# Performance work log

Hardware: AMD Instinct MI355X
Metric: run time of the kernel (lower is better)

The kernel has to match this reference:

```python
import jax, jax.numpy as jnp
import numpy as np

EPS = 1e-08


def setup_inputs() -> dict:
    key = jax.random.key(0)
    student_output = jax.random.normal(key, (8192, 1024), dtype=jnp.float32)
    return {"student_output": student_output}


def reference(student_output) -> jnp.ndarray:
    # F.normalize(p=2, dim=-1, eps=EPS): x / max(||x||_2, eps)
    x = student_output.astype(jnp.float32)
    norm = jnp.linalg.norm(x, axis=-1, keepdims=True)
    x = x / jnp.maximum(norm, EPS)

    n = x.shape[0]
    # full similarity matrix with diagonal masked to -1.0 (self-sim excluded)
    sim = x @ x.T  # [N, N]
    sim = jnp.where(jnp.eye(n, dtype=bool), jnp.float32(-1.0), sim)
    indices = jnp.argmax(sim, axis=1)  # nearest neighbor per row

    # torch.nn.PairwiseDistance(2, eps): ||x1 - x2 + eps||_2 along feature dim
    diff = x - x[indices] + EPS
    distances = jnp.sqrt(jnp.sum(diff * diff, axis=-1))

    return -jnp.mean(jnp.log(distances + EPS))
```

## Files before the change

### kernel.cpp

```cpp
#include <hip/hip_runtime.h>
#include <stdint.h>

#define N 8192
#define DIM 1024
#define EPSF 1e-8f
#define BK 64
#define NBLK 64
#define NTRI 2080

typedef __attribute__((ext_vector_type(4))) float f32x4;
typedef __attribute__((ext_vector_type(8))) short s16x8;

__device__ inline unsigned short f2bf(float f) {
  unsigned u = __float_as_uint(f);
  unsigned r = (u + 0x7FFFu + ((u >> 16) & 1u)) >> 16;
  return (unsigned short)r;
}

__device__ inline unsigned encf(float f) {
  unsigned u = __float_as_uint(f);
  return (u & 0x80000000u) ? ~u : (u | 0x80000000u);
}

#define XB_OFF   0
#define INV_OFF  16777216
#define KEY_OFF  16809984
#define PART_OFF 16875520

__global__ __launch_bounds__(256)
void k_norm(const float* __restrict__ x, unsigned short* __restrict__ xb,
            float* __restrict__ invn, unsigned long long* __restrict__ keys) {
  int row = blockIdx.x, t = threadIdx.x;
  const float4* xr = (const float4*)(x + (size_t)row * DIM);
  float4 v = xr[t];
  float ss = v.x * v.x + v.y * v.y + v.z * v.z + v.w * v.w;
#pragma unroll
  for (int o = 32; o > 0; o >>= 1) ss += __shfl_down(ss, o, 64);
  __shared__ float red[4];
  __shared__ float sinv;
  if ((t & 63) == 0) red[t >> 6] = ss;
  __syncthreads();
  if (t == 0) {
    float s = red[0] + red[1] + red[2] + red[3];
    float inv = 1.0f / fmaxf(sqrtf(s), EPSF);
    sinv = inv;
    invn[row] = inv;
    keys[row] = 0ull;
  }
  __syncthreads();
  float inv = sinv;
  ushort4 o4;
  o4.x = f2bf(v.x * inv);
  o4.y = f2bf(v.y * inv);
  o4.z = f2bf(v.z * inv);
  o4.w = f2bf(v.w * inv);
  ((ushort4*)(xb + (size_t)row * DIM))[t] = o4;
}

__global__ __launch_bounds__(256)
void k_sim(const unsigned short* __restrict__ xb, unsigned long long* __restrict__ keys) {
  int b = blockIdx.x;
  int bi = (int)((129.0f - sqrtf(16641.0f - 8.0f * (float)b)) * 0.5f);
  while ((bi + 1) * (129 - (bi + 1)) / 2 <= b) ++bi;
  while (bi * (129 - bi) / 2 > b) --bi;
  int bj = bi + (b - bi * (129 - bi) / 2);

  __shared__ unsigned short sA[128 * BK];
  __shared__ unsigned short sB[128 * BK];
  const int t = threadIdx.x, lane = t & 63, wv = t >> 6;
  const int wr = wv >> 1, wc = wv & 1;
  const int hi = lane >> 4, lo = lane & 15;
  const int rowBase = bi * 128, colBase = bj * 128;

  const f32x4 fzero = {0.f, 0.f, 0.f, 0.f};
  f32x4 acc[4][4];
#pragma unroll
  for (int i = 0; i < 4; ++i)
#pragma unroll
    for (int j = 0; j < 4; ++j) acc[i][j] = fzero;

  const int w8 = wv * 8 + (lane >> 3);
  const int cch = lane & 7;

  for (int kt = 0; kt < DIM / BK; ++kt) {
    const unsigned short* gA = xb + (size_t)rowBase * DIM + kt * BK;
    const unsigned short* gB = xb + (size_t)colBase * DIM + kt * BK;
#pragma unroll
    for (int rd = 0; rd < 4; ++rd) {
      int r = rd * 32 + w8;
      int c = cch ^ (r & 7);
      __builtin_amdgcn_global_load_lds(
          (const __attribute__((address_space(1))) void*)(gA + (size_t)r * DIM + c * 8),
          (__attribute__((address_space(3))) void*)(&sA[rd * 2048 + wv * 512]),
          16, 0, 0);
      __builtin_amdgcn_global_load_lds(
          (const __attribute__((address_space(1))) void*)(gB + (size_t)r * DIM + c * 8),
          (__attribute__((address_space(3))) void*)(&sB[rd * 2048 + wv * 512]),
          16, 0, 0);
    }
    __syncthreads();
#pragma unroll
    for (int kk = 0; kk < 2; ++kk) {
      s16x8 af[4], bf[4];
#pragma unroll
      for (int mi = 0; mi < 4; ++mi) {
        int r = wr * 64 + mi * 16 + lo;
        int c = (kk * 4 + hi) ^ (r & 7);
        af[mi] = *(const s16x8*)(&sA[r * BK + c * 8]);
      }
#pragma unroll
      for (int ni = 0; ni < 4; ++ni) {
        int r = wc * 64 + ni * 16 + lo;
        int c = (kk * 4 + hi) ^ (r & 7);
        bf[ni] = *(const s16x8*)(&sB[r * BK + c * 8]);
      }
#pragma unroll
      for (int mi = 0; mi < 4; ++mi)
#pragma unroll
        for (int ni = 0; ni < 4; ++ni)
          acc[mi][ni] = __builtin_amdgcn_mfma_f32_16x16x32_bf16(af[mi], bf[ni], acc[mi][ni], 0, 0, 0);
    }
    __syncthreads();
  }

#pragma unroll
  for (int mi = 0; mi < 4; ++mi) {
#pragma unroll
    for (int reg = 0; reg < 4; ++reg) {
      int grow = rowBase + wr * 64 + mi * 16 + hi * 4 + reg;
      float best = -10.0f;
      int bcol = 0;
#pragma unroll
      for (int ni = 0; ni < 4; ++ni) {
        int gcol = colBase + wc * 64 + ni * 16 + lo;
        float v = acc[mi][ni][reg];
        v = (gcol == grow) ? -10.0f : v;
        if (v > best || (v == best && gcol < bcol)) { best = v; bcol = gcol; }
      }
#pragma unroll
      for (int m = 1; m < 16; m <<= 1) {
        float ov = __shfl_xor(best, m, 64);
        int oc = __shfl_xor(bcol, m, 64);
        if (ov > best || (ov == best && oc < bcol)) { best = ov; bcol = oc; }
      }
      if (lo == 0) {
        unsigned long long key = ((unsigned long long)encf(best) << 32) | (unsigned)(~bcol);
        atomicMax(&keys[grow], key);
      }
    }
  }

  if (bi != bj) {
#pragma unroll
    for (int ni = 0; ni < 4; ++ni) {
      int gcol = colBase + wc * 64 + ni * 16 + lo;
      float best = -10.0f;
      int brow = 0;
#pragma unroll
      for (int mi = 0; mi < 4; ++mi)
#pragma unroll
        for (int reg = 0; reg < 4; ++reg) {
          int grow = rowBase + wr * 64 + mi * 16 + hi * 4 + reg;
          float v = acc[mi][ni][reg];
          if (v > best || (v == best && grow < brow)) { best = v; brow = grow; }
        }
#pragma unroll
      for (int m = 16; m < 64; m <<= 1) {
        float ov = __shfl_xor(best, m, 64);
        int oc = __shfl_xor(brow, m, 64);
        if (ov > best || (ov == best && oc < brow)) { best = ov; brow = oc; }
      }
      if (hi == 0) {
        unsigned long long key = ((unsigned long long)encf(best) << 32) | (unsigned)(~brow);
        atomicMax(&keys[gcol], key);
      }
    }
  }
}

__global__ __launch_bounds__(256)
void k_dist(const float* __restrict__ x, const float* __restrict__ invn,
            const unsigned long long* __restrict__ keys, float* __restrict__ part) {
  int row = blockIdx.x, t = threadIdx.x;
  unsigned long long key = keys[row];
  int nb = (int)(~(unsigned)key);
  float ia = invn[row], ib = invn[nb];
  float4 a = ((const float4*)(x + (size_t)row * DIM))[t];
  float4 b = ((const float4*)(x + (size_t)nb * DIM))[t];
  float d0 = a.x * ia - b.x * ib + EPSF;
  float d1 = a.y * ia - b.y * ib + EPSF;
  float d2 = a.z * ia - b.z * ib + EPSF;
  float d3 = a.w * ia - b.w * ib + EPSF;
  float ss = d0 * d0 + d1 * d1 + d2 * d2 + d3 * d3;
#pragma unroll
  for (int o = 32; o > 0; o >>= 1) ss += __shfl_down(ss, o, 64);
  __shared__ float red[4];
  if ((t & 63) == 0) red[t >> 6] = ss;
  __syncthreads();
  if (t == 0) {
    float s = red[0] + red[1] + red[2] + red[3];
    part[row] = logf(sqrtf(s) + EPSF);
  }
}

__global__ __launch_bounds__(1024)
void k_final(const float* __restrict__ part, float* __restrict__ out) {
  int t = threadIdx.x;
  float s = 0.0f;
#pragma unroll
  for (int i = 0; i < N / 1024; ++i) s += part[t + i * 1024];
#pragma unroll
  for (int o = 32; o > 0; o >>= 1) s += __shfl_down(s, o, 64);
  __shared__ float red[16];
  if ((t & 63) == 0) red[t >> 6] = s;
  __syncthreads();
  if (t == 0) {
    float tot = 0.0f;
#pragma unroll
    for (int i = 0; i < 16; ++i) tot += red[i];
    out[0] = -tot / (float)N;
  }
}

extern "C" void kernel_launch(void* const* d_in, const int* in_sizes, int n_in,
                              void* d_out, int out_size, void* d_ws, size_t ws_size,
                              hipStream_t stream) {
  const float* x = (const float*)d_in[0];
  float* out = (float*)d_out;
  char* ws = (char*)d_ws;
  unsigned short* xb = (unsigned short*)(ws + XB_OFF);
  float* invn = (float*)(ws + INV_OFF);
  unsigned long long* keys = (unsigned long long*)(ws + KEY_OFF);
  float* part = (float*)(ws + PART_OFF);

  k_norm<<<N, 256, 0, stream>>>(x, xb, invn, keys);
  k_sim<<<NTRI, 256, 0, stream>>>(xb, keys);
  k_dist<<<N, 256, 0, stream>>>(x, invn, keys, part);
  k_final<<<1, 1024, 0, stream>>>(part, out);
}
```

Before: 245.0 us.

## Enlarge sim tiles to 256x256 with double-buffered LDS prefetch and 8 waves

The similarity kernel now uses 256x256 tiles over the upper triangle (528 blocks), 8 waves of 512 threads, and a BK=32 double-buffered LDS pipeline. Global-to-LDS loads for the next k-step are issued while MFMAs run on the current buffer, and s_setprio raises priority around the MFMA bursts. This targets load latency stalls and improves operand reuse per loaded byte. In exchange it raises register pressure from 32 accumulators per thread and adds more barriers, and with only 528 blocks the final wave of work may load the CUs unevenly.

```diff
diff --git a/kernel.cpp b/kernel.cpp
--- a/kernel.cpp
+++ b/kernel.cpp
@@ -4,9 +4,8 @@
 #define N 8192
 #define DIM 1024
 #define EPSF 1e-8f
-#define BK 64
-#define NBLK 64
-#define NTRI 2080
+#define NBLK 32
+#define NTRI 528
 
 typedef __attribute__((ext_vector_type(4))) float f32x4;
 typedef __attribute__((ext_vector_type(8))) short s16x8;
@@ -57,83 +56,117 @@
   ((ushort4*)(xb + (size_t)row * DIM))[t] = o4;
 }
 
-__global__ __launch_bounds__(256)
+__global__ __launch_bounds__(512, 2)
 void k_sim(const unsigned short* __restrict__ xb, unsigned long long* __restrict__ keys) {
   int b = blockIdx.x;
-  int bi = (int)((129.0f - sqrtf(16641.0f - 8.0f * (float)b)) * 0.5f);
-  while ((bi + 1) * (129 - (bi + 1)) / 2 <= b) ++bi;
-  while (bi * (129 - bi) / 2 > b) --bi;
-  int bj = bi + (b - bi * (129 - bi) / 2);
-
-  __shared__ unsigned short sA[128 * BK];
-  __shared__ unsigned short sB[128 * BK];
+  int bi = (int)((65.0f - sqrtf(4225.0f - 8.0f * (float)b)) * 0.5f);
+  while ((bi + 1) * (65 - (bi + 1)) / 2 <= b) ++bi;
+  while (bi * (65 - bi) / 2 > b) --bi;
+  int bj = bi + (b - bi * (65 - bi) / 2);
+
+  __shared__ unsigned short sA[2][8192];
+  __shared__ unsigned short sB[2][8192];
+
   const int t = threadIdx.x, lane = t & 63, wv = t >> 6;
-  const int wr = wv >> 1, wc = wv & 1;
+  const int wr = wv >> 2, wc = wv & 3;
   const int hi = lane >> 4, lo = lane & 15;
-  const int rowBase = bi * 128, colBase = bj * 128;
+  const int rowBase = bi * 256, colBase = bj * 256;
+
+  const unsigned short* gA = xb + (size_t)rowBase * DIM;
+  const unsigned short* gB = xb + (size_t)colBase * DIM;
+
+  const int sg = (lane & 3) ^ ((lane >> 3) & 3);
+  const int r0 = wv * 16 + (lane >> 2);
+  const size_t so0 = (size_t)r0 * DIM + sg * 8;
+  const size_t so1 = (size_t)(r0 + 128) * DIM + sg * 8;
+  const int lb0 = wv * 512;
+  const int lb1 = 4096 + wv * 512;
 
   const f32x4 fzero = {0.f, 0.f, 0.f, 0.f};
-  f32x4 acc[4][4];
-#pragma unroll
-  for (int i = 0; i < 4; ++i)
+  f32x4 acc[8][4];
+#pragma unroll
+  for (int i = 0; i < 8; ++i)
 #pragma unroll
     for (int j = 0; j < 4; ++j) acc[i][j] = fzero;
 
-  const int w8 = wv * 8 + (lane >> 3);
-  const int cch = lane & 7;
-
-  for (int kt = 0; kt < DIM / BK; ++kt) {
-    const unsigned short* gA = xb + (size_t)rowBase * DIM + kt * BK;
-    const unsigned short* gB = xb + (size_t)colBase * DIM + kt * BK;
-#pragma unroll
-    for (int rd = 0; rd < 4; ++rd) {
-      int r = rd * 32 + w8;
-      int c = cch ^ (r & 7);
-      __builtin_amdgcn_global_load_lds(
-          (const __attribute__((address_space(1))) void*)(gA + (size_t)r * DIM + c * 8),
-          (__attribute__((address_space(3))) void*)(&sA[rd * 2048 + wv * 512]),
-          16, 0, 0);
-      __builtin_amdgcn_global_load_lds(
-          (const __attribute__((address_space(1))) void*)(gB + (size_t)r * DIM + c * 8),
-          (__attribute__((address_space(3))) void*)(&sB[rd * 2048 + wv * 512]),
-          16, 0, 0);
-    }
-    __syncthreads();
-#pragma unroll
-    for (int kk = 0; kk < 2; ++kk) {
-      s16x8 af[4], bf[4];
-#pragma unroll
-      for (int mi = 0; mi < 4; ++mi) {
-        int r = wr * 64 + mi * 16 + lo;
-        int c = (kk * 4 + hi) ^ (r & 7);
-        af[mi] = *(const s16x8*)(&sA[r * BK + c * 8]);
-      }
-#pragma unroll
-      for (int ni = 0; ni < 4; ++ni) {
-        int r = wc * 64 + ni * 16 + lo;
-        int c = (kk * 4 + hi) ^ (r & 7);
-        bf[ni] = *(const s16x8*)(&sB[r * BK + c * 8]);
-      }
-#pragma unroll
-      for (int mi = 0; mi < 4; ++mi)
-#pragma unroll
-        for (int ni = 0; ni < 4; ++ni)
-          acc[mi][ni] = __builtin_amdgcn_mfma_f32_16x16x32_bf16(af[mi], bf[ni], acc[mi][ni], 0, 0, 0);
-    }
-    __syncthreads();
-  }
-
-#pragma unroll
-  for (int mi = 0; mi < 4; ++mi) {
+  const int sr8 = (hi ^ ((lo >> 1) & 3)) * 8;
+
+  __builtin_amdgcn_global_load_lds((const __attribute__((address_space(1))) void*)(gA + so0),
+                                   (__attribute__((address_space(3))) void*)(&sA[0][lb0]), 16, 0, 0);
+  __builtin_amdgcn_global_load_lds((const __attribute__((address_space(1))) void*)(gA + so1),
+                                   (__attribute__((address_space(3))) void*)(&sA[0][lb1]), 16, 0, 0);
+  __builtin_amdgcn_global_load_lds((const __attribute__((address_space(1))) void*)(gB + so0),
+                                   (__attribute__((address_space(3))) void*)(&sB[0][lb0]), 16, 0, 0);
+  __builtin_amdgcn_global_load_lds((const __attribute__((address_space(1))) void*)(gB + so1),
+                                   (__attribute__((address_space(3))) void*)(&sB[0][lb1]), 16, 0, 0);
+  asm volatile("s_waitcnt vmcnt(0)" ::: "memory");
+  __builtin_amdgcn_s_barrier();
+
+  for (int kt = 0; kt < 32; ++kt) {
+    const int cur = kt & 1, nxt = cur ^ 1;
+    const size_t ko = (size_t)(kt + 1) * 32;
+    s16x8 af[4], bf[4];
+
+    if (kt < 31) {
+      __builtin_amdgcn_global_load_lds((const __attribute__((address_space(1))) void*)(gA + so0 + ko),
+                                       (__attribute__((address_space(3))) void*)(&sA[nxt][lb0]), 16, 0, 0);
+      __builtin_amdgcn_global_load_lds((const __attribute__((address_space(1))) void*)(gA + so1 + ko),
+                                       (__attribute__((address_space(3))) void*)(&sA[nxt][lb1]), 16, 0, 0);
+    }
+#pragma unroll
+    for (int mi = 0; mi < 4; ++mi) {
+      int r = wr * 128 + mi * 16 + lo;
+      af[mi] = *(const s16x8*)(&sA[cur][r * 32 + sr8]);
+    }
+#pragma unroll
+    for (int ni = 0; ni < 4; ++ni) {
+      int r = wc * 64 + ni * 16 + lo;
+      bf[ni] = *(const s16x8*)(&sB[cur][r * 32 + sr8]);
+    }
+    __builtin_amdgcn_s_barrier();
+    __builtin_amdgcn_s_setprio(1);
+#pragma unroll
+    for (int mi = 0; mi < 4; ++mi)
+#pragma unroll
+      for (int ni = 0; ni < 4; ++ni)
+        acc[mi][ni] = __builtin_amdgcn_mfma_f32_16x16x32_bf16(af[mi], bf[ni], acc[mi][ni], 0, 0, 0);
+    __builtin_amdgcn_s_setprio(0);
+    __builtin_amdgcn_s_barrier();
+
+    if (kt < 31) {
+      __builtin_amdgcn_global_load_lds((const __attribute__((address_space(1))) void*)(gB + so0 + ko),
+                                       (__attribute__((address_space(3))) void*)(&sB[nxt][lb0]), 16, 0, 0);
+      __builtin_amdgcn_global_load_lds((const __attribute__((address_space(1))) void*)(gB + so1 + ko),
+                                       (__attribute__((address_space(3))) void*)(&sB[nxt][lb1]), 16, 0, 0);
+    }
+#pragma unroll
+    for (int mi = 0; mi < 4; ++mi) {
+      int r = wr * 128 + 64 + mi * 16 + lo;
+      af[mi] = *(const s16x8*)(&sA[cur][r * 32 + sr8]);
+    }
+    __builtin_amdgcn_s_barrier();
+    __builtin_amdgcn_s_setprio(1);
+#pragma unroll
+    for (int mi = 0; mi < 4; ++mi)
+#pragma unroll
+      for (int ni = 0; ni < 4; ++ni)
+        acc[4 + mi][ni] = __builtin_amdgcn_mfma_f32_16x16x32_bf16(af[mi], bf[ni], acc[4 + mi][ni], 0, 0, 0);
+    __builtin_amdgcn_s_setprio(0);
+    asm volatile("s_waitcnt vmcnt(0)" ::: "memory");
+    __builtin_amdgcn_s_barrier();
+  }
+
+#pragma unroll
+  for (int am = 0; am < 8; ++am) {
 #pragma unroll
     for (int reg = 0; reg < 4; ++reg) {
-      int grow = rowBase + wr * 64 + mi * 16 + hi * 4 + reg;
+      int grow = rowBase + wr * 128 + am * 16 + hi * 4 + reg;
       float best = -10.0f;
       int bcol = 0;
 #pragma unroll
       for (int ni = 0; ni < 4; ++ni) {
         int gcol = colBase + wc * 64 + ni * 16 + lo;
-        float v = acc[mi][ni][reg];
+        float v = acc[am][ni][reg];
         v = (gcol == grow) ? -10.0f : v;
         if (v > best || (v == best && gcol < bcol)) { best = v; bcol = gcol; }
       }
@@ -157,11 +190,11 @@
       float best = -10.0f;
       int brow = 0;
 #pragma unroll
-      for (int mi = 0; mi < 4; ++mi)
+      for (int am = 0; am < 8; ++am)
 #pragma unroll
         for (int reg = 0; reg < 4; ++reg) {
-          int grow = rowBase + wr * 64 + mi * 16 + hi * 4 + reg;
-          float v = acc[mi][ni][reg];
+          int grow = rowBase + wr * 128 + am * 16 + hi * 4 + reg;
+          float v = acc[am][ni][reg];
           if (v > best || (v == best && grow < brow)) { best = v; brow = grow; }
         }
 #pragma unroll
@@ -234,7 +267,7 @@
   float* part = (float*)(ws + PART_OFF);
 
   k_norm<<<N, 256, 0, stream>>>(x, xb, invn, keys);
-  k_sim<<<NTRI, 256, 0, stream>>>(xb, keys);
+  k_sim<<<NTRI, 512, 0, stream>>>(xb, keys);
   k_dist<<<N, 256, 0, stream>>>(x, invn, keys, part);
   k_final<<<1, 1024, 0, stream>>>(part, out);
 }
```

Result: slower. 279.3 us (+14.0%).
